# Optimization experiments

Measured on AMD Instinct MI355X. Metric: run time of the kernel, lower is better.

The kernel has to match this reference:

```python
import jax, jax.numpy as jnp
import numpy as np

V, D, H, DFF, L = 32000, 256, 4, 1024, 4
B, T = 2, 2048
DK = D // H
EPS = 1e-5


def setup_inputs() -> dict:
    key = jax.random.key(0)
    ks = jax.random.split(key, 8)
    s = 0.02
    return {
        "tokens": jax.random.randint(ks[0], (B, T), 0, V),
        "embed": jax.random.normal(ks[1], (V, D), jnp.float32) * s,
        "qkv_w": jax.random.normal(ks[2], (L, 3 * D, D), jnp.float32) * s,
        "qkv_b": jnp.zeros((L, 3 * D), jnp.float32),
        "fc_w": jax.random.normal(ks[3], (L, D, D), jnp.float32) * s,
        "fc_b": jnp.zeros((L, D), jnp.float32),
        "ln1_s": jnp.ones((L, D), jnp.float32),
        "ln1_b": jnp.zeros((L, D), jnp.float32),
        "w1": jax.random.normal(ks[4], (L, DFF, D), jnp.float32) * s,
        "b1": jnp.zeros((L, DFF), jnp.float32),
        "w2": jax.random.normal(ks[5], (L, D, DFF), jnp.float32) * s,
        "b2": jnp.zeros((L, D), jnp.float32),
        "ln2_s": jnp.ones((L, D), jnp.float32),
        "ln2_b": jnp.zeros((L, D), jnp.float32),
        "lnf_s": jnp.ones((D,), jnp.float32),
        "lnf_b": jnp.zeros((D,), jnp.float32),
        "out_w": jax.random.normal(ks[6], (V, D), jnp.float32) * s,
        "out_b": jnp.zeros((V,), jnp.float32),
    }


def _layernorm(x, s, b):
    mu = jnp.mean(x, axis=-1, keepdims=True)
    var = jnp.mean(jnp.square(x - mu), axis=-1, keepdims=True)
    return (x - mu) * jax.lax.rsqrt(var + EPS) * s + b


def _pos_encoding(t, d):
    pos = jnp.arange(t, dtype=jnp.float32)[:, None]
    div = jnp.exp(jnp.arange(0, d, 2, dtype=jnp.float32) * (-np.log(10000.0) / d))
    pe = jnp.zeros((t, d), jnp.float32)
    pe = pe.at[:, 0::2].set(jnp.sin(pos * div))
    pe = pe.at[:, 1::2].set(jnp.cos(pos * div))
    return pe


def reference(tokens, embed, qkv_w, qkv_b, fc_w, fc_b, ln1_s, ln1_b,
              w1, b1, w2, b2, ln2_s, ln2_b, lnf_s, lnf_b, out_w, out_b):
    b, t = tokens.shape
    x = embed[tokens] + _pos_encoding(t, D)[None]  # [B,T,D]
    causal = jnp.tril(jnp.ones((t, t), bool))
    scale = 1.0 / np.sqrt(DK)
    for l in range(L):
        # --- attention ---
        qkv = jnp.einsum('btd,ed->bte', x, qkv_w[l]) + qkv_b[l]  # [B,T,3D]
        qkv = qkv.reshape(b, t, 3, H, DK)
        q, k, v = qkv[:, :, 0], qkv[:, :, 1], qkv[:, :, 2]  # [B,T,H,DK]
        scores = jnp.einsum('bqhd,bkhd->bhqk', q, k) * scale
        scores = jnp.where(causal, scores, -jnp.inf)
        attn = jax.nn.softmax(scores, axis=-1)
        o = jnp.einsum('bhqk,bkhd->bqhd', attn, v).reshape(b, t, D)
        o = jnp.einsum('btd,ed->bte', o, fc_w[l]) + fc_b[l]
        x = _layernorm(x + o, ln1_s[l], ln1_b[l])
        # --- feed-forward ---
        h = jax.nn.relu(jnp.einsum('btd,fd->btf', x, w1[l]) + b1[l])
        f = jnp.einsum('btf,df->btd', h, w2[l]) + b2[l]
        x = _layernorm(x + f, ln2_s[l], ln2_b[l])
    x = _layernorm(x, lnf_s, lnf_b)
    logits = jnp.einsum('btd,vd->btv', x, out_w) + out_b
    return logits
```

## Files before the change

### kernel.cpp

```cpp
#include <hip/hip_runtime.h>
#include <math.h>

typedef __attribute__((ext_vector_type(8))) short bf16x8;
typedef __attribute__((ext_vector_type(4))) float f32x4;
typedef __attribute__((ext_vector_type(4))) unsigned int u32x4;
typedef __attribute__((ext_vector_type(4))) unsigned short u16x4;

static constexpr int Tn = 2048;
static constexpr int Dm = 256;
static constexpr int NHn = 4;
static constexpr int Ln = 4;
static constexpr int DFFn = 1024;
static constexpr int Vn = 32000;
static constexpr int BTn = 4096;

__device__ __forceinline__ unsigned short f2bf(float f) {
  unsigned int u = __float_as_uint(f);
  u += 0x7fffu + ((u >> 16) & 1u);
  return (unsigned short)(u >> 16);
}

__global__ __launch_bounds__(256) void cvt_all(const float* __restrict__ s0, unsigned short* __restrict__ d0,
                                               const float* __restrict__ s1, unsigned short* __restrict__ d1,
                                               const float* __restrict__ s2, unsigned short* __restrict__ d2,
                                               const float* __restrict__ s3, unsigned short* __restrict__ d3,
                                               const float* __restrict__ s4, unsigned short* __restrict__ d4,
                                               int e0, int e1, int e2, int e3, int e4) {
  int g = blockIdx.x * 256 + threadIdx.x;
  if (g >= e4) return;
  const float* s; unsigned short* d; int base;
  if (g < e0)      { s = s0; d = d0; base = 0; }
  else if (g < e1) { s = s1; d = d1; base = e0; }
  else if (g < e2) { s = s2; d = d2; base = e1; }
  else if (g < e3) { s = s3; d = d3; base = e2; }
  else             { s = s4; d = d4; base = e3; }
  int i = (g - base) * 4;
  float4 v = *reinterpret_cast<const float4*>(s + i);
  u16x4 o;
  o[0] = f2bf(v.x); o[1] = f2bf(v.y); o[2] = f2bf(v.z); o[3] = f2bf(v.w);
  *reinterpret_cast<u16x4*>(d + i) = o;
}

__global__ __launch_bounds__(256) void embed_pos(const int* __restrict__ tokens,
                                                 const float* __restrict__ emb,
                                                 float* __restrict__ xf,
                                                 unsigned short* __restrict__ xb) {
  int idx = blockIdx.x * 256 + threadIdx.x;
  int bt = idx >> 8, d = idx & 255;
  int t = bt & (Tn - 1);
  int tok = tokens[bt];
  float v = emb[(size_t)tok * Dm + d];
  int i2 = d & ~1;
  float dv = expf((float)i2 * (-0.03597789207803249f));
  float arg = (float)t * dv;
  float pe = (d & 1) ? cosf(arg) : sinf(arg);
  float x = v + pe;
  xf[idx] = x;
  xb[idx] = f2bf(x);
}

__global__ __launch_bounds__(256) void add_ln(const float* __restrict__ addend,
                                              const float* __restrict__ gam,
                                              const float* __restrict__ bet,
                                              float* __restrict__ xf,
                                              unsigned short* __restrict__ xb) {
  int row = blockIdx.x, d = threadIdx.x;
  __shared__ float red[8];
  size_t off = (size_t)row * Dm + d;
  float u = xf[off];
  if (addend) u += addend[off];
  float tsum = u;
  #pragma unroll
  for (int o = 32; o > 0; o >>= 1) tsum += __shfl_xor(tsum, o);
  int w = d >> 6, lane = d & 63;
  if (lane == 0) red[w] = tsum;
  __syncthreads();
  float mean = (red[0] + red[1] + red[2] + red[3]) * (1.f / 256.f);
  float df = u - mean;
  float vsum = df * df;
  #pragma unroll
  for (int o = 32; o > 0; o >>= 1) vsum += __shfl_xor(vsum, o);
  if (lane == 0) red[4 + w] = vsum;
  __syncthreads();
  float var = (red[4] + red[5] + red[6] + red[7]) * (1.f / 256.f);
  float y = df * rsqrtf(var + 1e-5f) * gam[d] + bet[d];
  xf[off] = y;
  xb[off] = f2bf(y);
}

__global__ __launch_bounds__(256) void attn_mfma(const unsigned short* __restrict__ qkv,
                                                 unsigned short* __restrict__ ob) {
  int lin = blockIdx.y * gridDim.x + blockIdx.x;
  int wg = (lin & 7) * 32 + (lin >> 3);
  int qb = wg & 31, bh = wg >> 5;
  int b = bh >> 2, h = bh & 3;
  int q0 = qb * 64;
  int tid = threadIdx.x;
  int lane = tid & 63, w = tid >> 6;
  int l15 = lane & 15, quad = lane >> 4;

  __shared__ __align__(16) unsigned short Ps[4][16 * 64];
  __shared__ __align__(16) unsigned short Vt[64 * 64];

  const size_t rowQ = (size_t)(b * Tn + q0 + w * 16 + l15) * 768 + h * 64 + quad * 8;
  bf16x8 aq0 = *reinterpret_cast<const bf16x8*>(qkv + rowQ);
  bf16x8 aq1 = *reinterpret_cast<const bf16x8*>(qkv + rowQ + 32);

  float m_i[4], l_i[4];
  f32x4 oacc[4];
  #pragma unroll
  for (int i = 0; i < 4; i++) { m_i[i] = -INFINITY; l_i[i] = 0.f; oacc[i] = (f32x4){0.f, 0.f, 0.f, 0.f}; }

  for (int jt = 0; jt <= qb; jt++) {
    int j0 = jt * 64;
    __syncthreads();
    {
      int kv = tid & 63, g = tid >> 6;
      const unsigned short* vsrc = qkv + (size_t)(b * Tn + j0 + kv) * 768 + 512 + h * 64 + g * 16;
      bf16x8 v0 = *reinterpret_cast<const bf16x8*>(vsrc);
      bf16x8 v1 = *reinterpret_cast<const bf16x8*>(vsrc + 8);
      char* vb = (char*)Vt;
      #pragma unroll
      for (int j = 0; j < 8; j++) {
        int dk = g * 16 + j;
        *(unsigned short*)(vb + (((dk * 128 + kv * 2)) ^ ((dk & 7) << 4))) = (unsigned short)v0[j];
      }
      #pragma unroll
      for (int j = 0; j < 8; j++) {
        int dk = g * 16 + 8 + j;
        *(unsigned short*)(vb + (((dk * 128 + kv * 2)) ^ ((dk & 7) << 4))) = (unsigned short)v1[j];
      }
    }
    __syncthreads();

    f32x4 sc[4];
    const size_t rowK = (size_t)(b * Tn + j0 + l15) * 768 + 256 + h * 64 + quad * 8;
    #pragma unroll
    for (int f = 0; f < 4; f++) {
      bf16x8 bk0 = *reinterpret_cast<const bf16x8*>(qkv + rowK + (size_t)f * 16 * 768);
      bf16x8 bk1 = *reinterpret_cast<const bf16x8*>(qkv + rowK + (size_t)f * 16 * 768 + 32);
      f32x4 a = (f32x4){0.f, 0.f, 0.f, 0.f};
      a = __builtin_amdgcn_mfma_f32_16x16x32_bf16(aq0, bk0, a, 0, 0, 0);
      a = __builtin_amdgcn_mfma_f32_16x16x32_bf16(aq1, bk1, a, 0, 0, 0);
      sc[f] = a;
    }

    bool diag = (jt == qb);
    float alpha[4];
    #pragma unroll
    for (int rr = 0; rr < 4; rr++) {
      int qg = q0 + w * 16 + quad * 4 + rr;
      float sv[4];
      #pragma unroll
      for (int f = 0; f < 4; f++) {
        sv[f] = sc[f][rr] * 0.125f;
        if (diag && (j0 + f * 16 + l15 > qg)) sv[f] = -INFINITY;
      }
      float mx = fmaxf(fmaxf(sv[0], sv[1]), fmaxf(sv[2], sv[3]));
      #pragma unroll
      for (int o = 8; o > 0; o >>= 1) mx = fmaxf(mx, __shfl_xor(mx, o));
      float mnew = fmaxf(m_i[rr], mx);
      float p[4], ps = 0.f;
      #pragma unroll
      for (int f = 0; f < 4; f++) { p[f] = __expf(sv[f] - mnew); ps += p[f]; }
      #pragma unroll
      for (int o = 8; o > 0; o >>= 1) ps += __shfl_xor(ps, o);
      alpha[rr] = __expf(m_i[rr] - mnew);
      l_i[rr] = l_i[rr] * alpha[rr] + ps;
      m_i[rr] = mnew;
      int qq = quad * 4 + rr;
      char* pb = (char*)Ps[w];
      #pragma unroll
      for (int f = 0; f < 4; f++)
        *(unsigned short*)(pb + (((qq * 128 + (f * 16 + l15) * 2)) ^ ((qq & 7) << 4))) = f2bf(p[f]);
    }

    #pragma unroll
    for (int ni = 0; ni < 4; ni++)
      #pragma unroll
      for (int rr = 0; rr < 4; rr++) oacc[ni][rr] *= alpha[rr];

    bf16x8 pa[2];
    {
      char* pb = (char*)Ps[w];
      #pragma unroll
      for (int kc = 0; kc < 2; kc++)
        pa[kc] = *reinterpret_cast<const bf16x8*>(
            pb + (((l15 * 128 + kc * 64 + quad * 16)) ^ ((l15 & 7) << 4)));
    }
    char* vb = (char*)Vt;
    #pragma unroll
    for (int ni = 0; ni < 4; ni++) {
      int dk = ni * 16 + l15;
      #pragma unroll
      for (int kc = 0; kc < 2; kc++) {
        bf16x8 bv = *reinterpret_cast<const bf16x8*>(
            vb + (((dk * 128 + kc * 64 + quad * 16)) ^ ((dk & 7) << 4)));
        oacc[ni] = __builtin_amdgcn_mfma_f32_16x16x32_bf16(pa[kc], bv, oacc[ni], 0, 0, 0);
      }
    }
  }

  #pragma unroll
  for (int ni = 0; ni < 4; ni++) {
    #pragma unroll
    for (int rr = 0; rr < 4; rr++) {
      int qg = q0 + w * 16 + quad * 4 + rr;
      float o = oacc[ni][rr] / l_i[rr];
      ob[(size_t)(b * Tn + qg) * Dm + h * 64 + ni * 16 + l15] = f2bf(o);
    }
  }
}

template <int BM, int K, int EPI>
__global__ __launch_bounds__(256) void gemm_rf(const unsigned short* __restrict__ A,
                                               const unsigned short* __restrict__ W,
                                               const float* __restrict__ bias,
                                               float* __restrict__ Cf,
                                               unsigned short* __restrict__ Cb,
                                               int N) {
  constexpr int MI = BM / 32;
  int tid = threadIdx.x;
  int lane = tid & 63, w = tid >> 6;
  int wm = (w >> 1) * (BM / 2), wn = (w & 1) * 64;
  int r = lane & 15, quad = lane >> 4;

  int gx = gridDim.x;
  int nwg = gx * gridDim.y;
  int lin = blockIdx.y * gx + blockIdx.x;
  int xcd = lin & 7, pos = lin >> 3;
  int qch = nwg >> 3, rch = nwg & 7;
  int wg = (xcd < rch ? xcd * (qch + 1) : rch * (qch + 1) + (xcd - rch) * qch) + pos;
  int m0 = (wg % gx) * BM;
  int n0 = (wg / gx) * 128;

  const unsigned short* Ap = A + (size_t)(m0 + wm + r) * K + quad * 8;
  const unsigned short* Wp = W + (size_t)(n0 + wn + r) * K + quad * 8;

  f32x4 acc[MI][4];
  #pragma unroll
  for (int i = 0; i < MI; i++)
    #pragma unroll
    for (int j = 0; j < 4; j++) acc[i][j] = (f32x4){0.f, 0.f, 0.f, 0.f};

  #pragma unroll 8
  for (int k0 = 0; k0 < K; k0 += 32) {
    bf16x8 af[MI], bfr[4];
    #pragma unroll
    for (int mi = 0; mi < MI; mi++)
      af[mi] = *reinterpret_cast<const bf16x8*>(Ap + (size_t)mi * 16 * K + k0);
    #pragma unroll
    for (int ni = 0; ni < 4; ni++)
      bfr[ni] = *reinterpret_cast<const bf16x8*>(Wp + (size_t)ni * 16 * K + k0);
    #pragma unroll
    for (int mi = 0; mi < MI; mi++)
      #pragma unroll
      for (int ni = 0; ni < 4; ni++)
        acc[mi][ni] = __builtin_amdgcn_mfma_f32_16x16x32_bf16(af[mi], bfr[ni], acc[mi][ni], 0, 0, 0);
  }

  #pragma unroll
  for (int mi = 0; mi < MI; mi++) {
    #pragma unroll
    for (int ni = 0; ni < 4; ni++) {
      int n = n0 + wn + ni * 16 + r;
      float bv = bias[n];
      #pragma unroll
      for (int rr = 0; rr < 4; rr++) {
        int m = m0 + wm + mi * 16 + quad * 4 + rr;
        float v = acc[mi][ni][rr] + bv;
        if (EPI == 0) {
          Cf[(size_t)m * N + n] = v;
        } else if (EPI == 1) {
          Cb[(size_t)m * N + n] = f2bf(fmaxf(v, 0.f));
        } else {
          Cb[(size_t)m * N + n] = f2bf(v);
        }
      }
    }
  }
}

extern "C" void kernel_launch(void* const* d_in, const int* in_sizes, int n_in,
                              void* d_out, int out_size, void* d_ws, size_t ws_size,
                              hipStream_t stream) {
  (void)in_sizes; (void)n_in; (void)out_size; (void)ws_size;
  const int* tokens = (const int*)d_in[0];
  const float* emb = (const float*)d_in[1];
  const float* qkv_w = (const float*)d_in[2];
  const float* qkv_b = (const float*)d_in[3];
  const float* fc_w = (const float*)d_in[4];
  const float* fc_b = (const float*)d_in[5];
  const float* ln1_s = (const float*)d_in[6];
  const float* ln1_b = (const float*)d_in[7];
  const float* w1 = (const float*)d_in[8];
  const float* b1 = (const float*)d_in[9];
  const float* w2 = (const float*)d_in[10];
  const float* b2 = (const float*)d_in[11];
  const float* ln2_s = (const float*)d_in[12];
  const float* ln2_b = (const float*)d_in[13];
  const float* lnf_s = (const float*)d_in[14];
  const float* lnf_b = (const float*)d_in[15];
  const float* out_w = (const float*)d_in[16];
  const float* out_b = (const float*)d_in[17];
  float* logits = (float*)d_out;

  char* p = (char*)d_ws;
  auto carve = [&](size_t bytes) {
    char* r = p;
    p += (bytes + 255) & ~(size_t)255;
    return r;
  };
  float* xf = (float*)carve((size_t)BTn * Dm * 4);
  unsigned short* xb = (unsigned short*)carve((size_t)BTn * Dm * 2);
  unsigned short* qkvb = (unsigned short*)carve((size_t)BTn * 768 * 2);
  unsigned short* obb = (unsigned short*)carve((size_t)BTn * Dm * 2);
  float* of = (float*)carve((size_t)BTn * Dm * 4);
  unsigned short* hb = (unsigned short*)carve((size_t)BTn * DFFn * 2);
  float* ff = (float*)carve((size_t)BTn * Dm * 4);
  unsigned short* wqkvb = (unsigned short*)carve((size_t)Ln * 768 * Dm * 2);
  unsigned short* wfcb = (unsigned short*)carve((size_t)Ln * Dm * Dm * 2);
  unsigned short* w1b = (unsigned short*)carve((size_t)Ln * DFFn * Dm * 2);
  unsigned short* w2b = (unsigned short*)carve((size_t)Ln * Dm * DFFn * 2);
  unsigned short* outwb = (unsigned short*)carve((size_t)Vn * Dm * 2);

  {
    int c0 = Ln * 768 * Dm / 4;
    int c1 = c0 + Ln * Dm * Dm / 4;
    int c2 = c1 + Ln * DFFn * Dm / 4;
    int c3 = c2 + Ln * Dm * DFFn / 4;
    int c4 = c3 + Vn * Dm / 4;
    cvt_all<<<dim3((c4 + 255) / 256), dim3(256), 0, stream>>>(
        qkv_w, wqkvb, fc_w, wfcb, w1, w1b, w2, w2b, out_w, outwb, c0, c1, c2, c3, c4);
  }

  embed_pos<<<dim3(BTn), dim3(256), 0, stream>>>(tokens, emb, xf, xb);

  for (int l = 0; l < Ln; l++) {
    gemm_rf<64, 256, 2><<<dim3(BTn / 64, 768 / 128), dim3(256), 0, stream>>>(
        xb, wqkvb + (size_t)l * 768 * Dm, qkv_b + l * 768, nullptr, qkvb, 768);
    attn_mfma<<<dim3(Tn / 64, 2 * NHn), dim3(256), 0, stream>>>(qkvb, obb);
    gemm_rf<32, 256, 0><<<dim3(BTn / 32, Dm / 128), dim3(256), 0, stream>>>(
        obb, wfcb + (size_t)l * Dm * Dm, fc_b + l * Dm, of, nullptr, Dm);
    add_ln<<<dim3(BTn), dim3(256), 0, stream>>>(of, ln1_s + l * Dm, ln1_b + l * Dm, xf, xb);
    gemm_rf<64, 256, 1><<<dim3(BTn / 64, DFFn / 128), dim3(256), 0, stream>>>(
        xb, w1b + (size_t)l * DFFn * Dm, b1 + l * DFFn, nullptr, hb, DFFn);
    gemm_rf<32, 1024, 0><<<dim3(BTn / 32, Dm / 128), dim3(256), 0, stream>>>(
        hb, w2b + (size_t)l * Dm * DFFn, b2 + l * Dm, ff, nullptr, Dm);
    add_ln<<<dim3(BTn), dim3(256), 0, stream>>>(ff, ln2_s + l * Dm, ln2_b + l * Dm, xf, xb);
  }
  add_ln<<<dim3(BTn), dim3(256), 0, stream>>>(nullptr, lnf_s, lnf_b, xf, xb);

  gemm_rf<128, 256, 0><<<dim3(BTn / 128, Vn / 128), dim3(256), 0, stream>>>(
      xb, outwb, out_b, logits, nullptr, Vn);
}
```

Baseline: 1.393 ms.

## Stage GEMM tiles through LDS and fuse output projections with residual LayerNorm

Replaces the register-direct GEMM with a double-buffered LDS version that uses global_load_lds async copies. It also adds a gemm_ln kernel that computes the fc and FFN-down projections over full 256-wide rows and applies bias, residual add and LayerNorm in the epilogue. This drops the separate add_ln launches and the fp32 intermediate buffers, and changes the FFN-up tile size to 128. In exchange, gemm_ln uses only 16 rows per block, so every block rereads the whole weight matrix, and each k-step now needs a barrier.

Result: faster. 1.204 ms (-13.6%).

```diff
diff --git a/kernel.cpp b/kernel.cpp
--- a/kernel.cpp
+++ b/kernel.cpp
@@ -18,6 +18,11 @@
   unsigned int u = __float_as_uint(f);
   u += 0x7fffu + ((u >> 16) & 1u);
   return (unsigned short)(u >> 16);
+}
+
+__device__ __forceinline__ void gld_lds16(const unsigned short* g, unsigned short* l) {
+  __builtin_amdgcn_global_load_lds((const __attribute__((address_space(1))) unsigned int*)g,
+                                   (__attribute__((address_space(3))) unsigned int*)l, 16, 0, 0);
 }
 
 __global__ __launch_bounds__(256) void cvt_all(const float* __restrict__ s0, unsigned short* __restrict__ d0,
@@ -212,14 +217,16 @@
   }
 }
 
-template <int BM, int K, int EPI>
-__global__ __launch_bounds__(256) void gemm_rf(const unsigned short* __restrict__ A,
+template <int BM, int EPI>
+__global__ __launch_bounds__(256) void gemm_bt(const unsigned short* __restrict__ A,
                                                const unsigned short* __restrict__ W,
                                                const float* __restrict__ bias,
                                                float* __restrict__ Cf,
                                                unsigned short* __restrict__ Cb,
-                                               int N) {
+                                               int M, int N, int K) {
   constexpr int MI = BM / 32;
+  __shared__ __align__(16) unsigned short As[2][BM * 32];
+  __shared__ __align__(16) unsigned short Bs[2][128 * 32];
   int tid = threadIdx.x;
   int lane = tid & 63, w = tid >> 6;
   int wm = (w >> 1) * (BM / 2), wn = (w & 1) * 64;
@@ -234,29 +241,46 @@
   int m0 = (wg % gx) * BM;
   int n0 = (wg / gx) * 128;
 
-  const unsigned short* Ap = A + (size_t)(m0 + wm + r) * K + quad * 8;
-  const unsigned short* Wp = W + (size_t)(n0 + wn + r) * K + quad * 8;
-
   f32x4 acc[MI][4];
   #pragma unroll
   for (int i = 0; i < MI; i++)
     #pragma unroll
     for (int j = 0; j < 4; j++) acc[i][j] = (f32x4){0.f, 0.f, 0.f, 0.f};
 
-  #pragma unroll 8
-  for (int k0 = 0; k0 < K; k0 += 32) {
+  int lrow = lane >> 2;
+  int lcol = (lane & 3) * 8;
+  auto STAGE = [&](int buf, int k0) {
+    #pragma unroll
+    for (int i = 0; i < BM / 64; i++) {
+      int rowA = i * 64 + w * 16;
+      gld_lds16(A + (size_t)(m0 + rowA + lrow) * K + k0 + lcol, &As[buf][rowA * 32]);
+    }
+    #pragma unroll
+    for (int i = 0; i < 2; i++) {
+      int rowB = i * 64 + w * 16;
+      gld_lds16(W + (size_t)(n0 + rowB + lrow) * K + k0 + lcol, &Bs[buf][rowB * 32]);
+    }
+  };
+
+  STAGE(0, 0);
+  __syncthreads();
+  int NT = K >> 5, cur = 0;
+  for (int t = 0; t < NT; t++) {
+    if (t + 1 < NT) STAGE(cur ^ 1, (t + 1) * 32);
     bf16x8 af[MI], bfr[4];
     #pragma unroll
     for (int mi = 0; mi < MI; mi++)
-      af[mi] = *reinterpret_cast<const bf16x8*>(Ap + (size_t)mi * 16 * K + k0);
+      af[mi] = *reinterpret_cast<const bf16x8*>(&As[cur][(wm + mi * 16 + r) * 32 + quad * 8]);
     #pragma unroll
     for (int ni = 0; ni < 4; ni++)
-      bfr[ni] = *reinterpret_cast<const bf16x8*>(Wp + (size_t)ni * 16 * K + k0);
+      bfr[ni] = *reinterpret_cast<const bf16x8*>(&Bs[cur][(wn + ni * 16 + r) * 32 + quad * 8]);
     #pragma unroll
     for (int mi = 0; mi < MI; mi++)
       #pragma unroll
       for (int ni = 0; ni < 4; ni++)
         acc[mi][ni] = __builtin_amdgcn_mfma_f32_16x16x32_bf16(af[mi], bfr[ni], acc[mi][ni], 0, 0, 0);
+    __syncthreads();
+    cur ^= 1;
   }
 
   #pragma unroll
@@ -277,6 +301,126 @@
           Cb[(size_t)m * N + n] = f2bf(v);
         }
       }
+    }
+  }
+}
+
+template <int K>
+__global__ __launch_bounds__(256) void gemm_ln(const unsigned short* __restrict__ A,
+                                               const unsigned short* __restrict__ W,
+                                               const float* __restrict__ bias,
+                                               const float* __restrict__ gam,
+                                               const float* __restrict__ bet,
+                                               float* __restrict__ xf,
+                                               unsigned short* __restrict__ xb) {
+  constexpr int NT = K / 32;
+  __shared__ __align__(16) unsigned short As[2][16 * 32];
+  __shared__ __align__(16) unsigned short Bs[2][256 * 32];
+  __shared__ float red0[4][16], red1[4][16];
+  int tid = threadIdx.x;
+  int lane = tid & 63, w = tid >> 6;
+  int l15 = lane & 15, quad = lane >> 4;
+  int m0 = blockIdx.x * 16;
+  int wn = w * 64;
+  int lrow = lane >> 2, lcol = (lane & 3) * 8;
+
+  f32x4 acc[4];
+  #pragma unroll
+  for (int i = 0; i < 4; i++) acc[i] = (f32x4){0.f, 0.f, 0.f, 0.f};
+
+  auto STAGE = [&](int buf, int k0) {
+    if (w == 0)
+      gld_lds16(A + (size_t)(m0 + lrow) * K + k0 + lcol, &As[buf][0]);
+    #pragma unroll
+    for (int i = 0; i < 4; i++) {
+      int rb = (i * 4 + w) * 16;
+      gld_lds16(W + (size_t)(rb + lrow) * K + k0 + lcol, &Bs[buf][rb * 32]);
+    }
+  };
+
+  STAGE(0, 0);
+  __syncthreads();
+  int cur = 0;
+  #pragma unroll 4
+  for (int t = 0; t < NT; t++) {
+    if (t + 1 < NT) STAGE(cur ^ 1, (t + 1) * 32);
+    bf16x8 af = *reinterpret_cast<const bf16x8*>(&As[cur][l15 * 32 + quad * 8]);
+    bf16x8 bfr[4];
+    #pragma unroll
+    for (int ni = 0; ni < 4; ni++)
+      bfr[ni] = *reinterpret_cast<const bf16x8*>(&Bs[cur][(wn + ni * 16 + l15) * 32 + quad * 8]);
+    #pragma unroll
+    for (int ni = 0; ni < 4; ni++)
+      acc[ni] = __builtin_amdgcn_mfma_f32_16x16x32_bf16(af, bfr[ni], acc[ni], 0, 0, 0);
+    __syncthreads();
+    cur ^= 1;
+  }
+
+  float v[4][4], s[4];
+  #pragma unroll
+  for (int rr = 0; rr < 4; rr++) s[rr] = 0.f;
+  #pragma unroll
+  for (int ni = 0; ni < 4; ni++) {
+    int n = wn + ni * 16 + l15;
+    float bv = bias[n];
+    #pragma unroll
+    for (int rr = 0; rr < 4; rr++) {
+      int m = m0 + quad * 4 + rr;
+      float x = acc[ni][rr] + bv + xf[(size_t)m * Dm + n];
+      v[ni][rr] = x;
+      s[rr] += x;
+    }
+  }
+  #pragma unroll
+  for (int rr = 0; rr < 4; rr++) {
+    #pragma unroll
+    for (int o = 8; o > 0; o >>= 1) s[rr] += __shfl_xor(s[rr], o);
+  }
+  if (l15 == 0) {
+    #pragma unroll
+    for (int rr = 0; rr < 4; rr++) red0[w][quad * 4 + rr] = s[rr];
+  }
+  __syncthreads();
+  float mean[4], vs[4];
+  #pragma unroll
+  for (int rr = 0; rr < 4; rr++) {
+    int rw = quad * 4 + rr;
+    mean[rr] = (red0[0][rw] + red0[1][rw] + red0[2][rw] + red0[3][rw]) * (1.f / 256.f);
+    vs[rr] = 0.f;
+  }
+  #pragma unroll
+  for (int ni = 0; ni < 4; ni++)
+    #pragma unroll
+    for (int rr = 0; rr < 4; rr++) {
+      float df = v[ni][rr] - mean[rr];
+      vs[rr] += df * df;
+    }
+  #pragma unroll
+  for (int rr = 0; rr < 4; rr++) {
+    #pragma unroll
+    for (int o = 8; o > 0; o >>= 1) vs[rr] += __shfl_xor(vs[rr], o);
+  }
+  if (l15 == 0) {
+    #pragma unroll
+    for (int rr = 0; rr < 4; rr++) red1[w][quad * 4 + rr] = vs[rr];
+  }
+  __syncthreads();
+  #pragma unroll
+  for (int rr = 0; rr < 4; rr++) {
+    int rw = quad * 4 + rr;
+    float var = (red1[0][rw] + red1[1][rw] + red1[2][rw] + red1[3][rw]) * (1.f / 256.f);
+    vs[rr] = rsqrtf(var + 1e-5f);
+  }
+  #pragma unroll
+  for (int ni = 0; ni < 4; ni++) {
+    int n = wn + ni * 16 + l15;
+    float g = gam[n], be = bet[n];
+    #pragma unroll
+    for (int rr = 0; rr < 4; rr++) {
+      int m = m0 + quad * 4 + rr;
+      float y = (v[ni][rr] - mean[rr]) * vs[rr] * g + be;
+      xf[(size_t)m * Dm + n] = y;
+      xb[(size_t)m * Dm + n] = f2bf(y);
     }
   }
 }
@@ -315,9 +459,7 @@
   unsigned short* xb = (unsigned short*)carve((size_t)BTn * Dm * 2);
   unsigned short* qkvb = (unsigned short*)carve((size_t)BTn * 768 * 2);
   unsigned short* obb = (unsigned short*)carve((size_t)BTn * Dm * 2);
-  float* of = (float*)carve((size_t)BTn * Dm * 4);
   unsigned short* hb = (unsigned short*)carve((size_t)BTn * DFFn * 2);
-  float* ff = (float*)carve((size_t)BTn * Dm * 4);
   unsigned short* wqkvb = (unsigned short*)carve((size_t)Ln * 768 * Dm * 2);
   unsigned short* wfcb = (unsigned short*)carve((size_t)Ln * Dm * Dm * 2);
   unsigned short* w1b = (unsigned short*)carve((size_t)Ln * DFFn * Dm * 2);
@@ -337,20 +479,18 @@
   embed_pos<<<dim3(BTn), dim3(256), 0, stream>>>(tokens, emb, xf, xb);
 
   for (int l = 0; l < Ln; l++) {
-    gemm_rf<64, 256, 2><<<dim3(BTn / 64, 768 / 128), dim3(256), 0, stream>>>(
-        xb, wqkvb + (size_t)l * 768 * Dm, qkv_b + l * 768, nullptr, qkvb, 768);
+    gemm_bt<64, 2><<<dim3(BTn / 64, 768 / 128), dim3(256), 0, stream>>>(
+        xb, wqkvb + (size_t)l * 768 * Dm, qkv_b + l * 768, nullptr, qkvb, BTn, 768, Dm);
     attn_mfma<<<dim3(Tn / 64, 2 * NHn), dim3(256), 0, stream>>>(qkvb, obb);
-    gemm_rf<32, 256, 0><<<dim3(BTn / 32, Dm / 128), dim3(256), 0, stream>>>(
-        obb, wfcb + (size_t)l * Dm * Dm, fc_b + l * Dm, of, nullptr, Dm);
-    add_ln<<<dim3(BTn), dim3(256), 0, stream>>>(of, ln1_s + l * Dm, ln1_b + l * Dm, xf, xb);
-    gemm_rf<64, 256, 1><<<dim3(BTn / 64, DFFn / 128), dim3(256), 0, stream>>>(
-        xb, w1b + (size_t)l * DFFn * Dm, b1 + l * DFFn, nullptr, hb, DFFn);
-    gemm_rf<32, 1024, 0><<<dim3(BTn / 32, Dm / 128), dim3(256), 0, stream>>>(
-        hb, w2b + (size_t)l * Dm * DFFn, b2 + l * Dm, ff, nullptr, Dm);
-    add_ln<<<dim3(BTn), dim3(256), 0, stream>>>(ff, ln2_s + l * Dm, ln2_b + l * Dm, xf, xb);
+    gemm_ln<256><<<dim3(BTn / 16), dim3(256), 0, stream>>>(
+        obb, wfcb + (size_t)l * Dm * Dm, fc_b + l * Dm, ln1_s + l * Dm, ln1_b + l * Dm, xf, xb);
+    gemm_bt<128, 1><<<dim3(BTn / 128, DFFn / 128), dim3(256), 0, stream>>>(
+        xb, w1b + (size_t)l * DFFn * Dm, b1 + l * DFFn, nullptr, hb, BTn, DFFn, Dm);
+    gemm_ln<1024><<<dim3(BTn / 16), dim3(256), 0, stream>>>(
+        hb, w2b + (size_t)l * Dm * DFFn, b2 + l * Dm, ln2_s + l * Dm, ln2_b + l * Dm, xf, xb);
   }
   add_ln<<<dim3(BTn), dim3(256), 0, stream>>>(nullptr, lnf_s, lnf_b, xf, xb);
 
-  gemm_rf<128, 256, 0><<<dim3(BTn / 128, Vn / 128), dim3(256), 0, stream>>>(
-      xb, outwb, out_b, logits, nullptr, Vn);
-}
+  gemm_bt<128, 0><<<dim3(BTn / 128, Vn / 128), dim3(256), 0, stream>>>(
+      xb, outwb, out_b, logits, nullptr, BTn, Vn, Dm);
+}
```
